# Kernel tuning notes

Measured on AMD Instinct MI355X. Metric: run time of the kernel, lower is better.

## Reference

```python
import math
import jax, jax.numpy as jnp
import numpy as np

B, S = 2, 2048
D, H, DK = 1024, 16, 64
M = 16            # nb_features
L = 4             # n_layers
DFF = 4096
VS, VT = 69, 69   # src/tgt vocab
NU = 10000        # num_users
FD = 34           # feature_dim
EPS = 1e-6


def make_pe(seq_len, d_model):
    pos = np.arange(seq_len, dtype=np.float32)[:, None]
    div = np.exp(np.arange(0, d_model, 2, dtype=np.float32) * (-math.log(10000.0) / d_model))
    pe = np.zeros((seq_len, d_model), np.float32)
    pe[:, 0::2] = np.sin(pos * div)
    pe[:, 1::2] = np.cos(pos * div)
    return jnp.asarray(pe)


def gelu_approx(x):
    return 0.5 * x * (1.0 + jnp.tanh(math.sqrt(2.0 / math.pi) * (x + 0.044715 * x ** 3)))


def layer_norm(x, alpha, bias):
    # torch LayerNormalization: unbiased std, eps added to std
    mu = x.mean(-1, keepdims=True)
    var = ((x - mu) ** 2).sum(-1, keepdims=True) / (x.shape[-1] - 1)
    return alpha * (x - mu) / (jnp.sqrt(var) + EPS) + bias


def setup_inputs():
    key = jax.random.key(0)
    ks = jax.random.split(key, 24)
    w = lambda k, shape, s=0.02: (jax.random.normal(k, shape, jnp.float32) * s)
    inp = {}
    inp['ids'] = jax.random.randint(ks[0], (B, S), 0, VS)
    inp['user_ids'] = jax.random.randint(ks[1], (B,), 0, NU)
    inp['id_embed'] = w(ks[2], (VS, D), 1.0)
    inp['feat_proj'] = w(ks[3], (D, FD))
    inp['gamma'] = jnp.float32(1.0)
    inp['gate_logits'] = w(ks[4], (NU, H))
    inp['wq'] = w(ks[5], (L, D, D))
    inp['wk'] = w(ks[6], (L, D, D))
    inp['wv'] = w(ks[7], (L, D, D))
    inp['wo'] = w(ks[8], (L, D, D))
    inp['omega'] = jax.random.normal(ks[9], (L, M, DK), jnp.float32) / math.sqrt(DK)
    inp['ln1_a'] = jnp.ones((L, D)); inp['ln1_b'] = jnp.zeros((L, D))
    inp['ln2_a'] = jnp.ones((L, D)); inp['ln2_b'] = jnp.zeros((L, D))
    inp['ff_w1'] = w(ks[10], (L, DFF, D)); inp['ff_b1'] = jnp.zeros((L, DFF))
    inp['ff_w2'] = w(ks[11], (L, D, DFF)); inp['ff_b2'] = jnp.zeros((L, D))
    inp['fin_a'] = jnp.ones((D,)); inp['fin_b'] = jnp.zeros((D,))
    inp['proj_w'] = w(ks[12], (VT, D)); inp['proj_b'] = jnp.zeros((VT,))
    inp['feat_tbl'] = w(ks[13], (VS, FD), 1.0)
    pm = np.zeros(VS, bool); pm[10:] = True   # ids >= 10 are products
    inp['prod_mask'] = jnp.asarray(pm)
    inp['pe'] = make_pe(S, D)
    return inp


def performer(xn, wq, wk, wv, wo, omega, gate):
    b, sq, _ = xn.shape
    q = (xn @ wq.T).reshape(b, sq, H, DK)
    k = (xn @ wk.T).reshape(b, sq, H, DK)
    v = (xn @ wv.T).reshape(b, sq, H, DK)
    # exp kernel feature map + row normalization
    qp = jnp.exp(-0.5 * (q @ omega.T) ** 2)        # (B,S,H,M)
    kp = jnp.exp(-0.5 * (k @ omega.T) ** 2)
    qp = qp / (qp.sum(-1, keepdims=True) + EPS)
    kp = kp / (kp.sum(-1, keepdims=True) + EPS)
    K_cum = jnp.cumsum(kp, axis=1)                              # (B,S,H,M)
    KV_cum = jnp.cumsum(kp[..., None] * v[..., None, :], axis=1)  # (B,S,H,M,DK)
    # blockwise causal index (block_size_h = block_size_w = 1)
    bh, bw = 1, 1
    ki = jnp.minimum((jnp.arange(sq) // bh + 1) * bw - 1, sq - 1)
    Ks = jnp.take(K_cum, ki, axis=1)
    KVs = jnp.take(KV_cum, ki, axis=1)
    num = jnp.einsum('bshm,bshmd->bshd', qp, KVs)
    den = jnp.sum(qp * Ks, -1, keepdims=True)
    out = num / (den + EPS)
    out = out * gate[:, None, :, None]
    return out.reshape(b, sq, D) @ wo.T


def reference(ids, user_ids, id_embed, feat_proj, gamma, gate_logits,
              wq, wk, wv, wo, omega, ln1_a, ln1_b, ln2_a, ln2_b,
              ff_w1, ff_b1, ff_w2, ff_b2, fin_a, fin_b,
              proj_w, proj_b, feat_tbl, prod_mask, pe):
    # SpecialPlusFeatureLookup
    id_vec = id_embed[ids]                       # (B,S,D)
    feat_vec = feat_tbl[ids] @ feat_proj.T       # (B,S,D)
    keep = prod_mask[ids]
    x = id_vec + gamma * (feat_vec * keep[..., None])
    # positional encoding (dropout=eval -> identity)
    x = x + pe[None, :x.shape[1], :]
    # per-user head gate
    gate = jax.nn.softmax(gate_logits[user_ids], axis=-1)  # (B,H)
    for l in range(L):
        x = x + performer(layer_norm(x, ln1_a[l], ln1_b[l]),
                          wq[l], wk[l], wv[l], wo[l], omega[l], gate)
        xn = layer_norm(x, ln2_a[l], ln2_b[l])
        x = x + (gelu_approx(xn @ ff_w1[l].T + ff_b1[l]) @ ff_w2[l].T + ff_b2[l])
    x = layer_norm(x, fin_a, fin_b)
    return x @ proj_w.T + proj_b                 # (B,S,VT)
```

## Files before the change

kernel.cpp:

```cpp
#include <hip/hip_runtime.h>
#include <hip/hip_bf16.h>
#include <math.h>

constexpr int BB  = 2;
constexpr int SS  = 2048;
constexpr int DD  = 1024;
constexpr int HH  = 16;
constexpr int DKK = 64;
constexpr int MB  = 16;
constexpr int LL  = 4;
constexpr int DF  = 4096;
constexpr int VSZ = 69;
constexpr int VTT = 69;
constexpr int FDD = 34;
constexpr float EPSF = 1e-6f;
constexpr int CL = 32;
constexpr int NC = SS / CL;

typedef unsigned short u16;
typedef unsigned int   u32;
using bf16x8 = __attribute__((ext_vector_type(8))) short;
using f32x4  = __attribute__((ext_vector_type(4))) float;

static __device__ __forceinline__ float b2f(u16 u) {
    union { u32 i; float f; } p; p.i = ((u32)u) << 16; return p.f;
}
static __device__ __forceinline__ u16 f2b(float f) {
    union { float f; u32 i; } p; p.f = f;
    u32 r = p.i + 0x7fffu + ((p.i >> 16) & 1u);
    return (u16)(r >> 16);
}
static __device__ __forceinline__ u32 pack2(float lo, float hi) {
    __hip_bfloat162 h = __float22bfloat162_rn(make_float2(lo, hi));
    return *(u32*)&h;
}
static __device__ __forceinline__ float gelu_f(float x) {
    float z = 0.7978845608028654f * (x + 0.044715f * x * x * x);
    z = fminf(fmaxf(z, -10.f), 10.f);
    float e = __expf(2.f * z);
    float th = (e - 1.f) / (e + 1.f);
    return 0.5f * x * (1.f + th);
}
static __device__ __forceinline__ float ldg1(const void* p, size_t i, int f32) {
    return f32 ? ((const float*)p)[i] : b2f(((const u16*)p)[i]);
}
static __device__ __forceinline__ float4 ldg4(const void* p, size_t i, int f32) {
    if (f32) return *(const float4*)((const float*)p + i);
    ushort4 u = *(const ushort4*)((const u16*)p + i);
    return make_float4(b2f(u.x), b2f(u.y), b2f(u.z), b2f(u.w));
}

#define GLD16(gp, lp) __builtin_amdgcn_global_load_lds( \
    (const __attribute__((address_space(1))) void*)(gp), \
    (__attribute__((address_space(3))) void*)(lp), 16, 0, 0)

__global__ void k_flag(const void* __restrict__ gamma, int* __restrict__ flag) {
    if (threadIdx.x == 0) *flag = (((const u16*)gamma)[0] == 0) ? 1 : 0;
}

__global__ __launch_bounds__(256) void k_build_tbl(
    const void* __restrict__ id_embed, const void* __restrict__ feat_tbl,
    const void* __restrict__ feat_proj, const void* __restrict__ gamma,
    const int* __restrict__ flagp, float* __restrict__ tbl)
{
    const int f32 = *flagp;
    int idx = blockIdx.x * 256 + threadIdx.x;
    if (idx >= VSZ * DD) return;
    int id = idx / DD, d = idx % DD;
    float acc = ldg1(id_embed, idx, f32);
    if (id >= 10) {
        float g = ldg1(gamma, 0, f32);
        float s = 0.f;
        for (int f = 0; f < FDD; ++f)
            s += ldg1(feat_tbl, (size_t)id * FDD + f, f32) * ldg1(feat_proj, (size_t)d * FDD + f, f32);
        acc += g * s;
    }
    tbl[idx] = acc;
}

__global__ __launch_bounds__(256) void k_gather(
    const float* __restrict__ tbl, const int* __restrict__ ids,
    const void* __restrict__ pe, const int* __restrict__ flagp, float* __restrict__ x)
{
    const int f32 = *flagp;
    int idx = blockIdx.x * 256 + threadIdx.x;
    int bs = idx >> 10, d = idx & (DD - 1);
    int s = bs & (SS - 1);
    x[idx] = tbl[ids[bs] * DD + d] + ldg1(pe, (size_t)s * DD + d, f32);
}

__global__ void k_gate(const void* __restrict__ gl, const int* __restrict__ uid,
                       const int* __restrict__ flagp, float* __restrict__ gate)
{
    const int f32 = *flagp;
    int b = threadIdx.x;
    if (b >= BB) return;
    size_t off = (size_t)uid[b] * HH;
    float v[HH], mx = -1e30f;
    for (int i = 0; i < HH; ++i) { v[i] = ldg1(gl, off + i, f32); mx = fmaxf(mx, v[i]); }
    float s = 0.f;
    for (int i = 0; i < HH; ++i) { v[i] = expf(v[i] - mx); s += v[i]; }
    for (int i = 0; i < HH; ++i) gate[b * HH + i] = v[i] / s;
}

__global__ __launch_bounds__(256) void k_layernorm(
    const float* __restrict__ x, const void* __restrict__ alpha,
    const void* __restrict__ beta, size_t p_off,
    const int* __restrict__ flagp, u16* __restrict__ y)
{
    const int f32 = *flagp;
    int row = blockIdx.x;
    const float* xr = x + (size_t)row * DD;
    int t = threadIdx.x;
    float v[4]; float s = 0.f;
    #pragma unroll
    for (int j = 0; j < 4; ++j) { v[j] = xr[t + j * 256]; s += v[j]; }
    __shared__ float red[8];
    int lane = t & 63, wv = t >> 6;
    #pragma unroll
    for (int off = 32; off > 0; off >>= 1) s += __shfl_down(s, off, 64);
    if (lane == 0) red[wv] = s;
    __syncthreads();
    float mu = (red[0] + red[1] + red[2] + red[3]) * (1.f / DD);
    __syncthreads();
    float ss = 0.f;
    #pragma unroll
    for (int j = 0; j < 4; ++j) { float dv = v[j] - mu; ss += dv * dv; }
    #pragma unroll
    for (int off = 32; off > 0; off >>= 1) ss += __shfl_down(ss, off, 64);
    if (lane == 0) red[wv] = ss;
    __syncthreads();
    float var = (red[0] + red[1] + red[2] + red[3]) * (1.f / (DD - 1));
    float rs = 1.f / (sqrtf(var) + EPSF);
    u16* yr = y + (size_t)row * DD;
    #pragma unroll
    for (int j = 0; j < 4; ++j) {
        int d = t + j * 256;
        yr[d] = f2b(ldg1(alpha, p_off + d, f32) * (v[j] - mu) * rs + ldg1(beta, p_off + d, f32));
    }
}

template<int BM, int BK>
static __device__ __forceinline__ void gemm_core(
    const u16* __restrict__ A, int lda,
    const void* __restrict__ W, size_t w_off, int ldw,
    const void* __restrict__ bias, size_t b_off, int f32,
    int K, int O, int act, int mode, u16* __restrict__ Cb, float* __restrict__ resid,
    int bx, int by)
{
    constexpr int NJ = (BM == 128) ? 4 : 2;
    constexpr int NP = BK / 32;
    __shared__ u16 As[NP * BM * 32];
    __shared__ u16 Bs[NP * 128 * 32];
    int t = threadIdx.x;
    int lane = t & 63, w = t >> 6;
    int quad = lane >> 4, l16 = lane & 15;
    int wm = (BM == 128) ? (w >> 1) * 64 : 0;
    int wn = (BM == 128) ? (w & 1) * 64 : w * 32;
    int n0 = by * BM, o0 = bx * 128;

    f32x4 acc[4][NJ];
    #pragma unroll
    for (int i = 0; i < 4; ++i)
        #pragma unroll
        for (int j = 0; j < NJ; ++j)
            #pragma unroll
            for (int r = 0; r < 4; ++r) acc[i][j][r] = 0.f;

    int r0 = t >> 2, c0 = (t & 3) * 8;
    const u16* Ap = A + (size_t)n0 * lda + c0;

    for (int k0 = 0; k0 < K; k0 += BK) {
        #pragma unroll
        for (int p = 0; p < NP; ++p) {
            int kk = k0 + p * 32;
            char* AsP = (char*)As + p * (BM * 64);
            char* BsP = (char*)Bs + p * 8192;
            GLD16(Ap + (size_t)r0 * lda + kk, AsP + t * 16);
            if (BM == 128)
                GLD16(Ap + (size_t)(r0 + 64) * lda + kk, AsP + 4096 + t * 16);
            if (f32) {
                const float* Wf = (const float*)W + w_off + kk + c0;
                const float* p0 = Wf + (size_t)(o0 + r0) * ldw;
                const float* p1 = p0 + (size_t)64 * ldw;
                float4 xa = *(const float4*)p0, xb = *(const float4*)(p0 + 4);
                uint4 pk;
                pk.x = pack2(xa.x, xa.y); pk.y = pack2(xa.z, xa.w);
                pk.z = pack2(xb.x, xb.y); pk.w = pack2(xb.z, xb.w);
                *(uint4*)(BsP + t * 16) = pk;
                float4 ya = *(const float4*)p1, yb = *(const float4*)(p1 + 4);
                pk.x = pack2(ya.x, ya.y); pk.y = pack2(ya.z, ya.w);
                pk.z = pack2(yb.x, yb.y); pk.w = pack2(yb.z, yb.w);
                *(uint4*)(BsP + 4096 + t * 16) = pk;
            } else {
                const u16* Wb = (const u16*)W + w_off + kk + c0;
                GLD16(Wb + (size_t)(o0 + r0) * ldw, BsP + t * 16);
                GLD16(Wb + (size_t)(o0 + r0 + 64) * ldw, BsP + 4096 + t * 16);
            }
        }
        __syncthreads();
        #pragma unroll
        for (int p = 0; p < NP; ++p) {
            const u16* AsP = As + p * (BM * 32);
            const u16* BsP = Bs + p * (128 * 32);
            bf16x8 af[4], bfv[NJ];
            #pragma unroll
            for (int i = 0; i < 4; ++i)
                af[i] = *(const bf16x8*)(AsP + (size_t)(wm + i * 16 + l16) * 32 + quad * 8);
            #pragma unroll
            for (int j = 0; j < NJ; ++j)
                bfv[j] = *(const bf16x8*)(BsP + (size_t)(wn + j * 16 + l16) * 32 + quad * 8);
            #pragma unroll
            for (int i = 0; i < 4; ++i)
                #pragma unroll
                for (int j = 0; j < NJ; ++j)
                    acc[i][j] = __builtin_amdgcn_mfma_f32_16x16x32_bf16(af[i], bfv[j], acc[i][j], 0, 0, 0);
        }
        __syncthreads();
    }
    #pragma unroll
    for (int i = 0; i < 4; ++i) {
        #pragma unroll
        for (int j = 0; j < NJ; ++j) {
            int col = o0 + wn + j * 16 + l16;
            float bval = bias ? ldg1(bias, b_off + col, f32) : 0.f;
            #pragma unroll
            for (int r = 0; r < 4; ++r) {
                int row = n0 + wm + i * 16 + quad * 4 + r;
                float val = acc[i][j][r] + bval;
                if (act) val = gelu_f(val);
                size_t idx = (size_t)row * O + col;
                if (mode == 1) resid[idx] += val;
                else           Cb[idx] = f2b(val);
            }
        }
    }
}

__global__ __launch_bounds__(256) void k_gemm128(
    const u16* __restrict__ A, int lda, const void* __restrict__ W, size_t w_off, int ldw,
    const void* __restrict__ bias, size_t b_off, const int* __restrict__ flagp,
    int K, int O, int act, int mode, u16* __restrict__ Cb, float* __restrict__ resid)
{
    gemm_core<128, 64>(A, lda, W, w_off, ldw, bias, b_off, *flagp, K, O, act, mode, Cb, resid,
                       blockIdx.x, blockIdx.y);
}

__global__ __launch_bounds__(256) void k_gemm64(
    const u16* __restrict__ A, int lda, const void* __restrict__ W, size_t w_off, int ldw,
    const void* __restrict__ bias, size_t b_off, const int* __restrict__ flagp,
    int K, int O, int act, int mode, u16* __restrict__ Cb, float* __restrict__ resid)
{
    gemm_core<64, 128>(A, lda, W, w_off, ldw, bias, b_off, *flagp, K, O, act, mode, Cb, resid,
                       blockIdx.x, blockIdx.y);
}

__global__ __launch_bounds__(256) void k_gemm_qkv(
    const u16* __restrict__ A,
    const void* __restrict__ Wq, const void* __restrict__ Wk, const void* __restrict__ Wv,
    size_t w_off, const int* __restrict__ flagp,
    u16* __restrict__ oq, u16* __restrict__ ok, u16* __restrict__ ov)
{
    const void* W = (blockIdx.z == 0) ? Wq : (blockIdx.z == 1) ? Wk : Wv;
    u16* o = (blockIdx.z == 0) ? oq : (blockIdx.z == 1) ? ok : ov;
    gemm_core<128, 64>(A, DD, W, w_off, DD, nullptr, 0, *flagp, DD, DD, 0, 0, o, nullptr,
                       blockIdx.x, blockIdx.y);
}

__global__ __launch_bounds__(256) void k_gemm_small(
    const u16* __restrict__ A, const void* __restrict__ W, size_t w_off, int ldw,
    const void* __restrict__ bias, size_t b_off,
    const int* __restrict__ flagp, int K, int O, void* __restrict__ outp)
{
    const int f32 = *flagp;
    __shared__ float As[16][68];
    __shared__ float Ws[16][68];
    int t = threadIdx.x;
    int tx = t & 15, ty = t >> 4;
    int o0 = blockIdx.x * 64, n0 = blockIdx.y * 64;
    int lr = t >> 2;
    int lk = (t & 3) * 4;
    float c[4][4] = {};
    for (int k0 = 0; k0 < K; k0 += 16) {
        ushort4 av = *(const ushort4*)(A + (size_t)(n0 + lr) * K + k0 + lk);
        As[lk + 0][lr] = b2f(av.x); As[lk + 1][lr] = b2f(av.y);
        As[lk + 2][lr] = b2f(av.z); As[lk + 3][lr] = b2f(av.w);
        float4 wv4 = make_float4(0.f, 0.f, 0.f, 0.f);
        int orow = o0 + lr;
        if (orow < O) wv4 = ldg4(W, w_off + (size_t)orow * ldw + k0 + lk, f32);
        Ws[lk + 0][lr] = wv4.x; Ws[lk + 1][lr] = wv4.y;
        Ws[lk + 2][lr] = wv4.z; Ws[lk + 3][lr] = wv4.w;
        __syncthreads();
        #pragma unroll
        for (int kk = 0; kk < 16; ++kk) {
            float4 a = *(const float4*)&As[kk][ty * 4];
            float4 b = *(const float4*)&Ws[kk][tx * 4];
            c[0][0] += a.x * b.x; c[0][1] += a.x * b.y; c[0][2] += a.x * b.z; c[0][3] += a.x * b.w;
            c[1][0] += a.y * b.x; c[1][1] += a.y * b.y; c[1][2] += a.y * b.z; c[1][3] += a.y * b.w;
            c[2][0] += a.z * b.x; c[2][1] += a.z * b.y; c[2][2] += a.z * b.z; c[2][3] += a.z * b.w;
            c[3][0] += a.w * b.x; c[3][1] += a.w * b.y; c[3][2] += a.w * b.z; c[3][3] += a.w * b.w;
        }
        __syncthreads();
    }
    #pragma unroll
    for (int i = 0; i < 4; ++i) {
        int n = n0 + ty * 4 + i;
        #pragma unroll
        for (int j = 0; j < 4; ++j) {
            int o = o0 + tx * 4 + j;
            if (o >= O) continue;
            float val = c[i][j];
            if (bias) val += ldg1(bias, b_off + o, f32);
            size_t idx = (size_t)n * O + o;
            if (f32) ((float*)outp)[idx] = val;
            else     ((u16*)outp)[idx] = f2b(val);
        }
    }
}

__global__ __launch_bounds__(256) void k_featmap(
    const u16* __restrict__ q, const void* __restrict__ omega, size_t o_off,
    const int* __restrict__ flagp, u16* __restrict__ qp_t)
{
    const int f32 = *flagp;
    __shared__ float q_s[64][68];
    __shared__ float om_s[16][68];
    int t = threadIdx.x;
    int bh = blockIdx.y, b = bh >> 4, h = bh & 15;
    int s0 = blockIdx.x * 64;
    const u16* qbase = q + (size_t)(b * SS + s0) * DD + h * DKK;
    #pragma unroll
    for (int i = 0; i < 2; ++i) {
        int idx = i * 256 + t;
        int si = idx >> 3, part = idx & 7;
        uint4 raw = *(const uint4*)(qbase + (size_t)si * DD + part * 8);
        const u16* pr = (const u16*)&raw;
        *(float4*)&q_s[si][part * 8]     = make_float4(b2f(pr[0]), b2f(pr[1]), b2f(pr[2]), b2f(pr[3]));
        *(float4*)&q_s[si][part * 8 + 4] = make_float4(b2f(pr[4]), b2f(pr[5]), b2f(pr[6]), b2f(pr[7]));
    }
    #pragma unroll
    for (int i = 0; i < 4; ++i) {
        int idx = i * 256 + t;
        om_s[idx >> 6][idx & 63] = ldg1(omega, o_off + idx, f32);
    }
    __syncthreads();
    int s = t >> 2, mg = t & 3;
    float u[4] = {0.f, 0.f, 0.f, 0.f};
    #pragma unroll
    for (int dk = 0; dk < 64; dk += 4) {
        float4 q4 = *(const float4*)&q_s[s][dk];
        #pragma unroll
        for (int mj = 0; mj < 4; ++mj) {
            float4 o4 = *(const float4*)&om_s[mg * 4 + mj][dk];
            u[mj] += q4.x * o4.x + q4.y * o4.y + q4.z * o4.z + q4.w * o4.w;
        }
    }
    float phi[4], tot = 0.f;
    #pragma unroll
    for (int mj = 0; mj < 4; ++mj) { phi[mj] = expf(-0.5f * u[mj] * u[mj]); tot += phi[mj]; }
    tot += __shfl_xor(tot, 1); tot += __shfl_xor(tot, 2);
    float inv = 1.f / (tot + EPSF);
    uint2 out;
    out.x = pack2(phi[0] * inv, phi[1] * inv);
    out.y = pack2(phi[2] * inv, phi[3] * inv);
    *(uint2*)(qp_t + ((size_t)bh * SS + s0 + s) * MB + mg * 4) = out;
}

__global__ __launch_bounds__(64) void k_scan_part(
    const u16* __restrict__ kp_t, const u16* __restrict__ v,
    float* __restrict__ kv_tot, float* __restrict__ kc_tot)
{
    int c = blockIdx.x, bh = blockIdx.y;
    int b = bh >> 4, h = bh & 15;
    int d = threadIdx.x;
    __shared__ float kp_s[CL * MB];
    const u16* kpb = kp_t + ((size_t)bh * SS + c * CL) * MB;
    #pragma unroll
    for (int i = 0; i < CL * MB / 64; ++i) {
        int idx = i * 64 + d;
        kp_s[idx] = b2f(kpb[idx]);
    }
    __syncthreads();
    float Kc[MB], KV[MB];
    #pragma unroll
    for (int m = 0; m < MB; ++m) { Kc[m] = 0.f; KV[m] = 0.f; }
    const u16* vp = v + ((size_t)b * SS + c * CL) * DD + h * DKK + d;
    for (int si = 0; si < CL; ++si) {
        float vd = b2f(vp[(size_t)si * DD]);
        #pragma unroll
        for (int m = 0; m < MB; ++m) {
            float kp = kp_s[si * MB + m];
            Kc[m] += kp; KV[m] += kp * vd;
        }
    }
    float* kvp = kv_tot + (((size_t)bh * NC + c) * MB) * DKK + d;
    #pragma unroll
    for (int m = 0; m < MB; ++m) kvp[(size_t)m * DKK] = KV[m];
    #pragma unroll
    for (int m = 0; m < MB; ++m)
        if (d == m) kc_tot[((size_t)bh * NC + c) * MB + m] = Kc[m];
}

__global__ __launch_bounds__(64) void k_scan_off(
    float* __restrict__ kv_tot, float* __restrict__ kc_tot)
{
    int bh = blockIdx.x; int d = threadIdx.x;
    if (d < MB) {
        float run = 0.f;
        for (int c = 0; c < NC; ++c) {
            size_t i = ((size_t)bh * NC + c) * MB + d;
            float tt = kc_tot[i]; kc_tot[i] = run; run += tt;
        }
    }
    float run[MB];
    #pragma unroll
    for (int m = 0; m < MB; ++m) run[m] = 0.f;
    for (int c = 0; c < NC; ++c) {
        size_t base = (((size_t)bh * NC + c) * MB) * DKK + d;
        float tt[MB];
        #pragma unroll
        for (int m = 0; m < MB; ++m) tt[m] = kv_tot[base + (size_t)m * DKK];
        #pragma unroll
        for (int m = 0; m < MB; ++m) { kv_tot[base + (size_t)m * DKK] = run[m]; run[m] += tt[m]; }
    }
}

__global__ __launch_bounds__(64) void k_scan_out(
    const u16* __restrict__ qp_t, const u16* __restrict__ kp_t, const u16* __restrict__ v,
    const float* __restrict__ kv_tot, const float* __restrict__ kc_tot,
    const float* __restrict__ gate, u16* __restrict__ attn)
{
    int c = blockIdx.x, bh = blockIdx.y;
    int b = bh >> 4, h = bh & 15;
    int d = threadIdx.x;
    __shared__ float kp_s[CL * MB], qp_s[CL * MB];
    const u16* kpb = kp_t + ((size_t)bh * SS + c * CL) * MB;
    const u16* qpb = qp_t + ((size_t)bh * SS + c * CL) * MB;
    #pragma unroll
    for (int i = 0; i < CL * MB / 64; ++i) {
        int idx = i * 64 + d;
        kp_s[idx] = b2f(kpb[idx]);
        qp_s[idx] = b2f(qpb[idx]);
    }
    __syncthreads();
    float Kc[MB], KV[MB];
    const float* kvp = kv_tot + (((size_t)bh * NC + c) * MB) * DKK + d;
    const float* kcp = kc_tot + ((size_t)bh * NC + c) * MB;
    #pragma unroll
    for (int m = 0; m < MB; ++m) { KV[m] = kvp[(size_t)m * DKK]; Kc[m] = kcp[m]; }
    float g = gate[bh];
    const u16* vp = v + ((size_t)b * SS + c * CL) * DD + h * DKK + d;
    u16* ap = attn + ((size_t)b * SS + c * CL) * DD + h * DKK + d;
    for (int si = 0; si < CL; ++si) {
        float vd = b2f(vp[(size_t)si * DD]);
        float num = 0.f, den = 0.f;
        #pragma unroll
        for (int m = 0; m < MB; ++m) {
            float kp = kp_s[si * MB + m];
            Kc[m] += kp; KV[m] += kp * vd;
            float qp = qp_s[si * MB + m];
            num += qp * KV[m]; den += qp * Kc[m];
        }
        ap[(size_t)si * DD] = f2b(num / (den + EPSF) * g);
    }
}

extern "C" void kernel_launch(void* const* d_in, const int* in_sizes, int n_in,
                              void* d_out, int out_size, void* d_ws, size_t ws_size,
                              hipStream_t stream)
{
    const int*  ids       = (const int*)d_in[0];
    const int*  user_ids  = (const int*)d_in[1];
    const void* id_embed  = d_in[2];
    const void* feat_proj = d_in[3];
    const void* gamma     = d_in[4];
    const void* gate_log  = d_in[5];
    const void* wq        = d_in[6];
    const void* wk        = d_in[7];
    const void* wv        = d_in[8];
    const void* wo        = d_in[9];
    const void* omega     = d_in[10];
    const void* ln1_a     = d_in[11];
    const void* ln1_b     = d_in[12];
    const void* ln2_a     = d_in[13];
    const void* ln2_b     = d_in[14];
    const void* ff_w1     = d_in[15];
    const void* ff_b1     = d_in[16];
    const void* ff_w2     = d_in[17];
    const void* ff_b2     = d_in[18];
    const void* fin_a     = d_in[19];
    const void* fin_b     = d_in[20];
    const void* proj_w    = d_in[21];
    const void* proj_b    = d_in[22];
    const void* feat_tbl  = d_in[23];
    const void* pe        = d_in[25];

    char* base = (char*)d_ws;
    const size_t MiB = (size_t)1 << 20;
    int*   flagp  = (int*)base;
    float* gate   = (float*)(base + 64);
    float* kc_tot = (float*)(base + 4096);
    float* tbl    = (float*)(base + 256 * 1024);
    float* x      = (float*)(base + 1 * MiB);
    u16*   xn     = (u16*)  (base + 17 * MiB);
    float* kv_tot = (float*)(base + 17 * MiB);
    u16*   qb     = (u16*)  (base + 25 * MiB);
    u16*   kb     = (u16*)  (base + 33 * MiB);
    u16*   vb     = (u16*)  (base + 41 * MiB);
    u16*   qp_t   = (u16*)  (base + 49 * MiB);
    u16*   kp_t   = (u16*)  (base + 51 * MiB);
    u16*   attn   = qb;
    u16*   ff1c   = qb;

    const int NT = BB * SS;

    k_flag<<<1, 64, 0, stream>>>(gamma, flagp);
    k_build_tbl<<<(VSZ * DD + 255) / 256, 256, 0, stream>>>(id_embed, feat_tbl, feat_proj, gamma, flagp, tbl);
    k_gather<<<(NT * DD) / 256, 256, 0, stream>>>(tbl, ids, pe, flagp, x);
    k_gate<<<1, 64, 0, stream>>>(gate_log, user_ids, flagp, gate);

    dim3 gQKV(DD / 128, NT / 128, 3);
    dim3 gWo(DD / 128, NT / 64);
    dim3 gF1(2048 / 128, NT / 128);
    dim3 gF2(DD / 128, NT / 64);
    dim3 gFeat(SS / 64, BB * HH);
    dim3 gScan(NC, BB * HH);

    for (int l = 0; l < LL; ++l) {
        size_t lDD = (size_t)l * DD * DD;
        k_layernorm<<<NT, 256, 0, stream>>>(x, ln1_a, ln1_b, (size_t)l * DD, flagp, xn);
        k_gemm_qkv<<<gQKV, 256, 0, stream>>>(xn, wq, wk, wv, lDD, flagp, qb, kb, vb);
        k_featmap<<<gFeat, 256, 0, stream>>>(qb, omega, (size_t)l * MB * DKK, flagp, qp_t);
        k_featmap<<<gFeat, 256, 0, stream>>>(kb, omega, (size_t)l * MB * DKK, flagp, kp_t);
        k_scan_part<<<gScan, 64, 0, stream>>>(kp_t, vb, kv_tot, kc_tot);
        k_scan_off<<<BB * HH, 64, 0, stream>>>(kv_tot, kc_tot);
        k_scan_out<<<gScan, 64, 0, stream>>>(qp_t, kp_t, vb, kv_tot, kc_tot, gate, attn);
        k_gemm64<<<gWo, 256, 0, stream>>>(attn, DD, wo, lDD, DD, nullptr, 0, flagp, DD, DD, 0, 1, nullptr, x);
        k_layernorm<<<NT, 256, 0, stream>>>(x, ln2_a, ln2_b, (size_t)l * DD, flagp, xn);
        for (int c = 0; c < 2; ++c) {
            size_t w1_off = (size_t)l * DF * DD + (size_t)c * 2048 * DD;
            size_t b1_off = (size_t)l * DF + c * 2048;
            size_t w2_off = (size_t)l * DD * DF + (size_t)c * 2048;
            k_gemm128<<<gF1, 256, 0, stream>>>(xn, DD, ff_w1, w1_off, DD, ff_b1, b1_off, flagp, DD, 2048, 1, 0, ff1c, nullptr);
            k_gemm64<<<gF2, 256, 0, stream>>>(ff1c, 2048, ff_w2, w2_off, DF,
                                              (c == 0) ? ff_b2 : nullptr, (size_t)l * DD,
                                              flagp, 2048, DD, 0, 1, nullptr, x);
        }
    }
    k_layernorm<<<NT, 256, 0, stream>>>(x, fin_a, fin_b, 0, flagp, xn);
    dim3 g4((VTT + 63) / 64, NT / 64);
    k_gemm_small<<<g4, 256, 0, stream>>>(xn, proj_w, 0, DD, proj_b, 0, flagp, DD, VTT, d_out);
}
```

Baseline: 1.912 ms.

## Double-buffer GEMM shared-memory tiles and halve K tile depth

Restructures the shared GEMM core into a two-stage ping-pong pipeline. The next K tile is loaded into the second LDS buffer while MFMAs run on the current one, and fp32 weights are held in registers before being packed into LDS after compute. The K tile size is halved for each kernel variant, so total LDS per block stays about the same. The aim is to hide global-load latency behind matrix math, at the cost of more registers and a main loop that assumes K/BK is even and at least 2.

```diff
diff --git a/kernel.cpp b/kernel.cpp
--- a/kernel.cpp
+++ b/kernel.cpp
@@ -148,10 +148,10 @@
     int K, int O, int act, int mode, u16* __restrict__ Cb, float* __restrict__ resid,
     int bx, int by)
 {
-    constexpr int NJ = (BM == 128) ? 4 : 2;
-    constexpr int NP = BK / 32;
-    __shared__ u16 As[NP * BM * 32];
-    __shared__ u16 Bs[NP * 128 * 32];
+    constexpr int NJ  = (BM == 128) ? 4 : 2;
+    constexpr int NPP = BK / 32;
+    __shared__ u16 As[2][NPP * BM * 32];
+    __shared__ u16 Bs[2][NPP * 128 * 32];
     int t = threadIdx.x;
     int lane = t & 63, w = t >> 6;
     int quad = lane >> 4, l16 = lane & 15;
@@ -169,55 +169,98 @@
 
     int r0 = t >> 2, c0 = (t & 3) * 8;
     const u16* Ap = A + (size_t)n0 * lda + c0;
-
-    for (int k0 = 0; k0 < K; k0 += BK) {
-        #pragma unroll
-        for (int p = 0; p < NP; ++p) {
-            int kk = k0 + p * 32;
-            char* AsP = (char*)As + p * (BM * 64);
-            char* BsP = (char*)Bs + p * 8192;
-            GLD16(Ap + (size_t)r0 * lda + kk, AsP + t * 16);
-            if (BM == 128)
-                GLD16(Ap + (size_t)(r0 + 64) * lda + kk, AsP + 4096 + t * 16);
-            if (f32) {
-                const float* Wf = (const float*)W + w_off + kk + c0;
-                const float* p0 = Wf + (size_t)(o0 + r0) * ldw;
-                const float* p1 = p0 + (size_t)64 * ldw;
-                float4 xa = *(const float4*)p0, xb = *(const float4*)(p0 + 4);
-                uint4 pk;
-                pk.x = pack2(xa.x, xa.y); pk.y = pack2(xa.z, xa.w);
-                pk.z = pack2(xb.x, xb.y); pk.w = pack2(xb.z, xb.w);
-                *(uint4*)(BsP + t * 16) = pk;
-                float4 ya = *(const float4*)p1, yb = *(const float4*)(p1 + 4);
-                pk.x = pack2(ya.x, ya.y); pk.y = pack2(ya.z, ya.w);
-                pk.z = pack2(yb.x, yb.y); pk.w = pack2(yb.z, yb.w);
-                *(uint4*)(BsP + 4096 + t * 16) = pk;
-            } else {
-                const u16* Wb = (const u16*)W + w_off + kk + c0;
-                GLD16(Wb + (size_t)(o0 + r0) * ldw, BsP + t * 16);
-                GLD16(Wb + (size_t)(o0 + r0 + 64) * ldw, BsP + 4096 + t * 16);
-            }
-        }
+    float4 wr[NPP][4];
+
+#define STAGE_A(IB, K0) do {                                                   \
+    _Pragma("unroll")                                                          \
+    for (int p = 0; p < NPP; ++p) {                                            \
+        int kk = (K0) + p * 32;                                                \
+        char* AsP = (char*)As[IB] + p * (BM * 64);                             \
+        GLD16(Ap + (size_t)r0 * lda + kk, AsP + t * 16);                       \
+        if (BM == 128)                                                         \
+            GLD16(Ap + (size_t)(r0 + 64) * lda + kk, AsP + 4096 + t * 16);     \
+    } } while (0)
+
+#define STAGE_WBF(IB, K0) do {                                                 \
+    _Pragma("unroll")                                                          \
+    for (int p = 0; p < NPP; ++p) {                                            \
+        int kk = (K0) + p * 32;                                                \
+        char* BsP = (char*)Bs[IB] + p * 8192;                                  \
+        const u16* Wb = (const u16*)W + w_off + kk + c0;                       \
+        GLD16(Wb + (size_t)(o0 + r0) * ldw, BsP + t * 16);                     \
+        GLD16(Wb + (size_t)(o0 + r0 + 64) * ldw, BsP + 4096 + t * 16);         \
+    } } while (0)
+
+#define LOADW_F32(K0) do {                                                     \
+    _Pragma("unroll")                                                          \
+    for (int p = 0; p < NPP; ++p) {                                            \
+        int kk = (K0) + p * 32;                                                \
+        const float* Wf = (const float*)W + w_off + kk + c0;                   \
+        const float* q0 = Wf + (size_t)(o0 + r0) * ldw;                        \
+        const float* q1 = q0 + (size_t)64 * ldw;                               \
+        wr[p][0] = *(const float4*)q0; wr[p][1] = *(const float4*)(q0 + 4);    \
+        wr[p][2] = *(const float4*)q1; wr[p][3] = *(const float4*)(q1 + 4);    \
+    } } while (0)
+
+#define WRITEW_F32(IB) do {                                                    \
+    _Pragma("unroll")                                                          \
+    for (int p = 0; p < NPP; ++p) {                                            \
+        char* BsP = (char*)Bs[IB] + p * 8192;                                  \
+        uint4 pk;                                                              \
+        pk.x = pack2(wr[p][0].x, wr[p][0].y); pk.y = pack2(wr[p][0].z, wr[p][0].w); \
+        pk.z = pack2(wr[p][1].x, wr[p][1].y); pk.w = pack2(wr[p][1].z, wr[p][1].w); \
+        *(uint4*)(BsP + t * 16) = pk;                                          \
+        pk.x = pack2(wr[p][2].x, wr[p][2].y); pk.y = pack2(wr[p][2].z, wr[p][2].w); \
+        pk.z = pack2(wr[p][3].x, wr[p][3].y); pk.w = pack2(wr[p][3].z, wr[p][3].w); \
+        *(uint4*)(BsP + 4096 + t * 16) = pk;                                   \
+    } } while (0)
+
+#define COMPUTE(IB) do {                                                       \
+    _Pragma("unroll")                                                          \
+    for (int p = 0; p < NPP; ++p) {                                            \
+        const u16* AsP = As[IB] + p * (BM * 32);                               \
+        const u16* BsP = Bs[IB] + p * (128 * 32);                              \
+        bf16x8 af[4], bfv[NJ];                                                 \
+        _Pragma("unroll")                                                      \
+        for (int i = 0; i < 4; ++i)                                            \
+            af[i] = *(const bf16x8*)(AsP + (size_t)(wm + i * 16 + l16) * 32 + quad * 8); \
+        _Pragma("unroll")                                                      \
+        for (int j = 0; j < NJ; ++j)                                           \
+            bfv[j] = *(const bf16x8*)(BsP + (size_t)(wn + j * 16 + l16) * 32 + quad * 8); \
+        _Pragma("unroll")                                                      \
+        for (int i = 0; i < 4; ++i)                                            \
+            _Pragma("unroll")                                                  \
+            for (int j = 0; j < NJ; ++j)                                       \
+                acc[i][j] = __builtin_amdgcn_mfma_f32_16x16x32_bf16(af[i], bfv[j], acc[i][j], 0, 0, 0); \
+    } } while (0)
+
+    const int nt = K / BK;
+    if (f32) { STAGE_A(0, 0); LOADW_F32(0); WRITEW_F32(0); }
+    else     { STAGE_A(0, 0); STAGE_WBF(0, 0); }
+    __syncthreads();
+
+    int k0 = BK;
+    for (int it = 0; it < nt / 2 - 1; ++it) {
+        if (f32) { STAGE_A(1, k0); LOADW_F32(k0); COMPUTE(0); WRITEW_F32(1); }
+        else     { STAGE_A(1, k0); STAGE_WBF(1, k0); COMPUTE(0); }
         __syncthreads();
-        #pragma unroll
-        for (int p = 0; p < NP; ++p) {
-            const u16* AsP = As + p * (BM * 32);
-            const u16* BsP = Bs + p * (128 * 32);
-            bf16x8 af[4], bfv[NJ];
-            #pragma unroll
-            for (int i = 0; i < 4; ++i)
-                af[i] = *(const bf16x8*)(AsP + (size_t)(wm + i * 16 + l16) * 32 + quad * 8);
-            #pragma unroll
-            for (int j = 0; j < NJ; ++j)
-                bfv[j] = *(const bf16x8*)(BsP + (size_t)(wn + j * 16 + l16) * 32 + quad * 8);
-            #pragma unroll
-            for (int i = 0; i < 4; ++i)
-                #pragma unroll
-                for (int j = 0; j < NJ; ++j)
-                    acc[i][j] = __builtin_amdgcn_mfma_f32_16x16x32_bf16(af[i], bfv[j], acc[i][j], 0, 0, 0);
-        }
+        k0 += BK;
+        if (f32) { STAGE_A(0, k0); LOADW_F32(k0); COMPUTE(1); WRITEW_F32(0); }
+        else     { STAGE_A(0, k0); STAGE_WBF(0, k0); COMPUTE(1); }
         __syncthreads();
-    }
+        k0 += BK;
+    }
+    if (f32) { STAGE_A(1, k0); LOADW_F32(k0); COMPUTE(0); WRITEW_F32(1); }
+    else     { STAGE_A(1, k0); STAGE_WBF(1, k0); COMPUTE(0); }
+    __syncthreads();
+    COMPUTE(1);
+
+#undef STAGE_A
+#undef STAGE_WBF
+#undef LOADW_F32
+#undef WRITEW_F32
+#undef COMPUTE
+
     #pragma unroll
     for (int i = 0; i < 4; ++i) {
         #pragma unroll
@@ -242,7 +285,7 @@
     const void* __restrict__ bias, size_t b_off, const int* __restrict__ flagp,
     int K, int O, int act, int mode, u16* __restrict__ Cb, float* __restrict__ resid)
 {
-    gemm_core<128, 64>(A, lda, W, w_off, ldw, bias, b_off, *flagp, K, O, act, mode, Cb, resid,
+    gemm_core<128, 32>(A, lda, W, w_off, ldw, bias, b_off, *flagp, K, O, act, mode, Cb, resid,
                        blockIdx.x, blockIdx.y);
 }
 
@@ -251,8 +294,8 @@
     const void* __restrict__ bias, size_t b_off, const int* __restrict__ flagp,
     int K, int O, int act, int mode, u16* __restrict__ Cb, float* __restrict__ resid)
 {
-    gemm_core<64, 128>(A, lda, W, w_off, ldw, bias, b_off, *flagp, K, O, act, mode, Cb, resid,
-                       blockIdx.x, blockIdx.y);
+    gemm_core<64, 64>(A, lda, W, w_off, ldw, bias, b_off, *flagp, K, O, act, mode, Cb, resid,
+                      blockIdx.x, blockIdx.y);
 }
 
 __global__ __launch_bounds__(256) void k_gemm_qkv(
@@ -263,7 +306,7 @@
 {
     const void* W = (blockIdx.z == 0) ? Wq : (blockIdx.z == 1) ? Wk : Wv;
     u16* o = (blockIdx.z == 0) ? oq : (blockIdx.z == 1) ? ok : ov;
-    gemm_core<128, 64>(A, DD, W, w_off, DD, nullptr, 0, *flagp, DD, DD, 0, 0, o, nullptr,
+    gemm_core<128, 32>(A, DD, W, w_off, DD, nullptr, 0, *flagp, DD, DD, 0, 0, o, nullptr,
                        blockIdx.x, blockIdx.y);
 }
 
```

Result: slower. 2.498 ms (+30.7%).

## Shrink GEMM tiles to 64 rows and remap blocks across XCDs

Applied to the files above, without the earlier changes.

Reworks the shared GEMM core so every block covers 64 rows and either 128 or 64 output columns, which doubles or quadruples the number of workgroups for the QKV, Wo, FF1 and FF2 GEMMs. It also adds an XCD-aware block index remap, so that consecutive tiles land on the same chiplet and its L2 is reused better. The aim is higher occupancy across the CUs and better cache locality. In exchange, each block does less compute per byte loaded, so total weight and activation traffic goes up.

```diff
diff --git a/kernel.cpp b/kernel.cpp
--- a/kernel.cpp
+++ b/kernel.cpp
@@ -140,7 +140,7 @@
     }
 }
 
-template<int BM, int BK>
+template<int BN, int BK>
 static __device__ __forceinline__ void gemm_core(
     const u16* __restrict__ A, int lda,
     const void* __restrict__ W, size_t w_off, int ldw,
@@ -148,80 +148,84 @@
     int K, int O, int act, int mode, u16* __restrict__ Cb, float* __restrict__ resid,
     int bx, int by)
 {
-    constexpr int NJ = (BM == 128) ? 4 : 2;
-    constexpr int NP = BK / 32;
-    __shared__ u16 As[NP * BM * 32];
-    __shared__ u16 Bs[NP * 128 * 32];
+    constexpr int NP  = BK / 32;
+    constexpr int NI  = (BN == 128) ? 4 : 2;
+    constexpr int WCOLS = (BN == 128) ? 4 : 2;
+    __shared__ u16 As[NP * 64 * 32];
+    __shared__ u16 Bs[NP * BN * 32];
     int t = threadIdx.x;
     int lane = t & 63, w = t >> 6;
     int quad = lane >> 4, l16 = lane & 15;
-    int wm = (BM == 128) ? (w >> 1) * 64 : 0;
-    int wn = (BM == 128) ? (w & 1) * 64 : w * 32;
-    int n0 = by * BM, o0 = bx * 128;
-
-    f32x4 acc[4][NJ];
-    #pragma unroll
-    for (int i = 0; i < 4; ++i)
-        #pragma unroll
-        for (int j = 0; j < NJ; ++j)
+    int wm = (w / WCOLS) * (NI * 16);
+    int wn = (w % WCOLS) * 32;
+    int n0 = by * 64, o0 = bx * BN;
+
+    f32x4 acc[NI][2];
+    #pragma unroll
+    for (int i = 0; i < NI; ++i)
+        #pragma unroll
+        for (int j = 0; j < 2; ++j)
             #pragma unroll
             for (int r = 0; r < 4; ++r) acc[i][j][r] = 0.f;
 
     int r0 = t >> 2, c0 = (t & 3) * 8;
     const u16* Ap = A + (size_t)n0 * lda + c0;
+    char* AsB = (char*)As;
+    char* BsB = (char*)Bs;
 
     for (int k0 = 0; k0 < K; k0 += BK) {
         #pragma unroll
         for (int p = 0; p < NP; ++p) {
             int kk = k0 + p * 32;
-            char* AsP = (char*)As + p * (BM * 64);
-            char* BsP = (char*)Bs + p * 8192;
+            char* AsP = AsB + p * 4096;
+            char* BsP = BsB + p * (BN * 64);
             GLD16(Ap + (size_t)r0 * lda + kk, AsP + t * 16);
-            if (BM == 128)
-                GLD16(Ap + (size_t)(r0 + 64) * lda + kk, AsP + 4096 + t * 16);
             if (f32) {
                 const float* Wf = (const float*)W + w_off + kk + c0;
-                const float* p0 = Wf + (size_t)(o0 + r0) * ldw;
-                const float* p1 = p0 + (size_t)64 * ldw;
-                float4 xa = *(const float4*)p0, xb = *(const float4*)(p0 + 4);
+                const float* q0 = Wf + (size_t)(o0 + r0) * ldw;
+                float4 xa = *(const float4*)q0, xb = *(const float4*)(q0 + 4);
                 uint4 pk;
                 pk.x = pack2(xa.x, xa.y); pk.y = pack2(xa.z, xa.w);
                 pk.z = pack2(xb.x, xb.y); pk.w = pack2(xb.z, xb.w);
                 *(uint4*)(BsP + t * 16) = pk;
-                float4 ya = *(const float4*)p1, yb = *(const float4*)(p1 + 4);
-                pk.x = pack2(ya.x, ya.y); pk.y = pack2(ya.z, ya.w);
-                pk.z = pack2(yb.x, yb.y); pk.w = pack2(yb.z, yb.w);
-                *(uint4*)(BsP + 4096 + t * 16) = pk;
+                if (BN == 128) {
+                    const float* q1 = q0 + (size_t)64 * ldw;
+                    float4 ya = *(const float4*)q1, yb = *(const float4*)(q1 + 4);
+                    pk.x = pack2(ya.x, ya.y); pk.y = pack2(ya.z, ya.w);
+                    pk.z = pack2(yb.x, yb.y); pk.w = pack2(yb.z, yb.w);
+                    *(uint4*)(BsP + 4096 + t * 16) = pk;
+                }
             } else {
                 const u16* Wb = (const u16*)W + w_off + kk + c0;
                 GLD16(Wb + (size_t)(o0 + r0) * ldw, BsP + t * 16);
-                GLD16(Wb + (size_t)(o0 + r0 + 64) * ldw, BsP + 4096 + t * 16);
+                if (BN == 128)
+                    GLD16(Wb + (size_t)(o0 + r0 + 64) * ldw, BsP + 4096 + t * 16);
             }
         }
         __syncthreads();
         #pragma unroll
         for (int p = 0; p < NP; ++p) {
-            const u16* AsP = As + p * (BM * 32);
-            const u16* BsP = Bs + p * (128 * 32);
-            bf16x8 af[4], bfv[NJ];
+            const u16* AsP = As + p * (64 * 32);
+            const u16* BsP = Bs + p * (BN * 32);
+            bf16x8 af[NI], bfv[2];
             #pragma unroll
-            for (int i = 0; i < 4; ++i)
+            for (int i = 0; i < NI; ++i)
                 af[i] = *(const bf16x8*)(AsP + (size_t)(wm + i * 16 + l16) * 32 + quad * 8);
             #pragma unroll
-            for (int j = 0; j < NJ; ++j)
+            for (int j = 0; j < 2; ++j)
                 bfv[j] = *(const bf16x8*)(BsP + (size_t)(wn + j * 16 + l16) * 32 + quad * 8);
             #pragma unroll
-            for (int i = 0; i < 4; ++i)
+            for (int i = 0; i < NI; ++i)
                 #pragma unroll
-                for (int j = 0; j < NJ; ++j)
+                for (int j = 0; j < 2; ++j)
                     acc[i][j] = __builtin_amdgcn_mfma_f32_16x16x32_bf16(af[i], bfv[j], acc[i][j], 0, 0, 0);
         }
         __syncthreads();
     }
     #pragma unroll
-    for (int i = 0; i < 4; ++i) {
-        #pragma unroll
-        for (int j = 0; j < NJ; ++j) {
+    for (int i = 0; i < NI; ++i) {
+        #pragma unroll
+        for (int j = 0; j < 2; ++j) {
             int col = o0 + wn + j * 16 + l16;
             float bval = bias ? ldg1(bias, b_off + col, f32) : 0.f;
             #pragma unroll
@@ -237,22 +241,33 @@
     }
 }
 
-__global__ __launch_bounds__(256) void k_gemm128(
+static __device__ __forceinline__ void xcd_tile(int& bx, int& by) {
+    int gx = gridDim.x;
+    int nwg = gx * gridDim.y;
+    int h = blockIdx.y * gx + blockIdx.x;
+    int q = nwg >> 3;
+    int lid = (h & 7) * q + (h >> 3);
+    bx = lid % gx; by = lid / gx;
+}
+
+__global__ __launch_bounds__(256) void k_gemm_a(
     const u16* __restrict__ A, int lda, const void* __restrict__ W, size_t w_off, int ldw,
     const void* __restrict__ bias, size_t b_off, const int* __restrict__ flagp,
     int K, int O, int act, int mode, u16* __restrict__ Cb, float* __restrict__ resid)
 {
+    int bx, by; xcd_tile(bx, by);
     gemm_core<128, 64>(A, lda, W, w_off, ldw, bias, b_off, *flagp, K, O, act, mode, Cb, resid,
-                       blockIdx.x, blockIdx.y);
-}
-
-__global__ __launch_bounds__(256) void k_gemm64(
+                       bx, by);
+}
+
+__global__ __launch_bounds__(256) void k_gemm_b(
     const u16* __restrict__ A, int lda, const void* __restrict__ W, size_t w_off, int ldw,
     const void* __restrict__ bias, size_t b_off, const int* __restrict__ flagp,
     int K, int O, int act, int mode, u16* __restrict__ Cb, float* __restrict__ resid)
 {
+    int bx, by; xcd_tile(bx, by);
     gemm_core<64, 128>(A, lda, W, w_off, ldw, bias, b_off, *flagp, K, O, act, mode, Cb, resid,
-                       blockIdx.x, blockIdx.y);
+                       bx, by);
 }
 
 __global__ __launch_bounds__(256) void k_gemm_qkv(
@@ -263,8 +278,9 @@
 {
     const void* W = (blockIdx.z == 0) ? Wq : (blockIdx.z == 1) ? Wk : Wv;
     u16* o = (blockIdx.z == 0) ? oq : (blockIdx.z == 1) ? ok : ov;
+    int bx, by; xcd_tile(bx, by);
     gemm_core<128, 64>(A, DD, W, w_off, DD, nullptr, 0, *flagp, DD, DD, 0, 0, o, nullptr,
-                       blockIdx.x, blockIdx.y);
+                       bx, by);
 }
 
 __global__ __launch_bounds__(256) void k_gemm_small(
@@ -519,10 +535,10 @@
     k_gather<<<(NT * DD) / 256, 256, 0, stream>>>(tbl, ids, pe, flagp, x);
     k_gate<<<1, 64, 0, stream>>>(gate_log, user_ids, flagp, gate);
 
-    dim3 gQKV(DD / 128, NT / 128, 3);
-    dim3 gWo(DD / 128, NT / 64);
-    dim3 gF1(2048 / 128, NT / 128);
-    dim3 gF2(DD / 128, NT / 64);
+    dim3 gQKV(DD / 128, NT / 64, 3);
+    dim3 gWo(DD / 64, NT / 64);
+    dim3 gF1(2048 / 128, NT / 64);
+    dim3 gF2(DD / 64, NT / 64);
     dim3 gFeat(SS / 64, BB * HH);
     dim3 gScan(NC, BB * HH);
 
@@ -535,14 +551,14 @@
         k_scan_part<<<gScan, 64, 0, stream>>>(kp_t, vb, kv_tot, kc_tot);
         k_scan_off<<<BB * HH, 64, 0, stream>>>(kv_tot, kc_tot);
         k_scan_out<<<gScan, 64, 0, stream>>>(qp_t, kp_t, vb, kv_tot, kc_tot, gate, attn);
-        k_gemm64<<<gWo, 256, 0, stream>>>(attn, DD, wo, lDD, DD, nullptr, 0, flagp, DD, DD, 0, 1, nullptr, x);
+        k_gemm_b<<<gWo, 256, 0, stream>>>(attn, DD, wo, lDD, DD, nullptr, 0, flagp, DD, DD, 0, 1, nullptr, x);
         k_layernorm<<<NT, 256, 0, stream>>>(x, ln2_a, ln2_b, (size_t)l * DD, flagp, xn);
         for (int c = 0; c < 2; ++c) {
             size_t w1_off = (size_t)l * DF * DD + (size_t)c * 2048 * DD;
             size_t b1_off = (size_t)l * DF + c * 2048;
             size_t w2_off = (size_t)l * DD * DF + (size_t)c * 2048;
-            k_gemm128<<<gF1, 256, 0, stream>>>(xn, DD, ff_w1, w1_off, DD, ff_b1, b1_off, flagp, DD, 2048, 1, 0, ff1c, nullptr);
-            k_gemm64<<<gF2, 256, 0, stream>>>(ff1c, 2048, ff_w2, w2_off, DF,
+            k_gemm_a<<<gF1, 256, 0, stream>>>(xn, DD, ff_w1, w1_off, DD, ff_b1, b1_off, flagp, DD, 2048, 1, 0, ff1c, nullptr);
+            k_gemm_b<<<gF2, 256, 0, stream>>>(ff1c, 2048, ff_w2, w2_off, DF,
                                               (c == 0) ? ff_b2 : nullptr, (size_t)l * DD,
                                               flagp, 2048, DD, 0, 1, nullptr, x);
         }
```

New measurement: 1.797 ms. 6.0% less time.
